# Kernel tuning notes

Measured on AMD Instinct MI355X. Metric: run time of the kernel, lower is better.

Reference implementation:

```python
import jax, jax.numpy as jnp
import numpy as np

B, H, N, T = 16, 16, 4096, 8
D_S, D_ID, L, K = 256, 128, 8, 32
HS, DQ = 8, 32
D_HID = 1024
D_STEER = 3 * D_S + D_ID  # cat(s_cur, id_cur, walker_state, token_embed)


def _gelu(x):
    return jax.nn.gelu(x, approximate=False)


def _rms(x, w):
    return x * jax.lax.rsqrt(jnp.mean(x * x, axis=-1, keepdims=True) + 1e-6) * w


def _mlp2(x, w1, b1, w2, b2):
    return _gelu(x @ w1 + b1) @ w2 + b2


def _per_plane_mlp(x, plane_idx, W1, b1, W2, b2):
    # x: [n, D_in]; plane_idx: [n] int in [0,L). Vectorized plane dispatch:
    # compute all planes then select (avoids data-dependent masking).
    h_all = jnp.einsum('nd,phd->nph', x, W1) + b1[None]          # [n,L,D_hid]
    h = jnp.take_along_axis(h_all, plane_idx[:, None, None], axis=1)[:, 0]
    h = _gelu(h)
    o_all = jnp.einsum('nh,pdh->npd', h, W2) + b2[None]          # [n,L,D_out]
    return jnp.take_along_axis(o_all, plane_idx[:, None, None], axis=1)[:, 0]


def setup_inputs() -> dict:
    key = jax.random.key(0)
    ks = jax.random.split(key, 16)
    f = jax.random.normal
    return {
        's': f(ks[0], (B, N, D_S), jnp.float32),
        'node_id': f(ks[1], (N, D_ID), jnp.float32),
        'walker_state': f(ks[2], (B, H, D_S), jnp.float32),
        'token_embed': f(ks[3], (B, T, D_S), jnp.float32),
        'norm_w': jnp.ones((D_S,), jnp.float32),
        'W1': f(ks[4], (L, D_HID, D_STEER), jnp.float32) * 0.014,
        'b1': jnp.zeros((L, D_HID), jnp.float32),
        'W2': f(ks[5], (L, D_S, D_HID), jnp.float32) * (2.0 / D_HID) ** 0.5,
        'b2': jnp.zeros((L, D_S), jnp.float32),
        'qw1': f(ks[6], (D_STEER, 2 * HS * DQ), jnp.float32) * 0.014,
        'qb1': jnp.zeros((2 * HS * DQ,), jnp.float32),
        'qw2': f(ks[7], (2 * HS * DQ, HS * DQ), jnp.float32) * 0.02,
        'qb2': jnp.zeros((HS * DQ,), jnp.float32),
        'kw1': f(ks[8], (D_ID, 2 * HS * DQ), jnp.float32) * 0.014,
        'kb1': jnp.zeros((2 * HS * DQ,), jnp.float32),
        'kw2': f(ks[9], (2 * HS * DQ, HS * DQ), jnp.float32) * 0.02,
        'kb2': jnp.zeros((HS * DQ,), jnp.float32),
        'walker_pos': jax.random.randint(ks[10], (B, H), 0, N, jnp.int32),
        'plane_idx': jax.random.randint(ks[11], (B, H), 0, L, jnp.int32),
        'neighbors': jax.random.randint(ks[12], (N, K), 0, N, jnp.int32),
    }


def reference(s, node_id, walker_state, token_embed, norm_w, W1, b1, W2, b2,
              qw1, qb1, qw2, qb2, kw1, kb1, kw2, kb2,
              walker_pos, plane_idx, neighbors):
    b_idx = jnp.arange(B)[:, None]            # [B,1] batch gather index
    plane_flat = plane_idx.reshape(-1)        # [B*H], constant per walker
    scale = 1.0 / (HS * np.sqrt(DQ).astype(np.float32))

    def step(carry, tok):
        s, pos, wstate, co, vc, lb = carry
        s_cur = s[b_idx, pos]                 # gather [B,H,D_s]
        id_cur = node_id[pos]                 # [B,H,D_id]
        s_n = _rms(s_cur, norm_w)
        tok_b = jnp.broadcast_to(tok[:, None, :], (B, H, D_S))
        steer = jnp.concatenate([s_n, id_cur, wstate, tok_b], axis=-1)  # [B,H,D_steer]
        # per-plane content MLP (dispatch by plane index)
        content = _per_plane_mlp(steer.reshape(B * H, D_STEER), plane_flat,
                                 W1, b1, W2, b2).reshape(B, H, D_S)
        # shared q/k projections and neighbor scoring
        q = _mlp2(steer, qw1, qb1, qw2, qb2).reshape(B, H, HS, DQ)
        nbr = neighbors[pos]                  # [B,H,K]
        k = _mlp2(node_id[nbr], kw1, kb1, kw2, kb2).reshape(B, H, K, HS, DQ)
        scores = jnp.einsum('bhsd,bhksd->bhk', q, k) * scale   # [B,H,K]
        probs = jax.nn.softmax(scores, axis=-1)
        mp = probs.mean(axis=(0, 1))
        lb = lb + K * jnp.sum(mp * mp)        # load-balance penalty
        # non-differentiable hop: argmax move
        sel = jnp.argmax(scores, axis=-1)     # [B,H]
        next_pos = jnp.take_along_axis(nbr, sel[..., None], axis=-1)[..., 0]
        # state updates: scatter content into s, residual walker state
        s_new = s.at[b_idx, pos].add(content)
        wstate_new = wstate + content
        # non-grad co-visit / visit-count accumulators
        pf = pos.reshape(-1)
        nf = next_pos.reshape(-1)
        co = co.at[pf, nf].add(1.0)
        vc = vc.at[nf].add(1.0)
        motor = wstate_new.mean(axis=1)       # [B,D_s]
        return (s_new, next_pos, wstate_new, co, vc, lb), motor

    init = (s, walker_pos, walker_state,
            jnp.zeros((N, N), jnp.float32), jnp.zeros((N,), jnp.float32),
            jnp.float32(0.0))
    (s_new, pos_new, ws_new, co, vc, lb), motors = jax.lax.scan(
        step, init, token_embed.transpose(1, 0, 2))
    motor_bt = motors.transpose(1, 0, 2)      # [B,T,D_s]
    return motor_bt, s_new, pos_new, ws_new, co, vc, lb
```

## Files before the change

### kernel.cpp

```cpp
#include <hip/hip_runtime.h>
#include <math.h>

#define B_    16
#define H_    16
#define N_    4096
#define T_    8
#define DS_   256
#define DID_  128
#define L_    8
#define K_    32
#define DHID_ 1024
#define DSTEER_ 896
#define QH_   512
#define QO_   256
#define NW_   256
#define SLOTS_ 512
#define SCORE_SCALE 0.022097086912079608f

struct KArgs {
    const float *s_in, *node_id, *ws_in, *token, *norm_w;
    const float *W1, *b1, *W2, *b2;
    const float *qw1, *qb1, *qw2, *qb2, *kw1, *kb1, *kw2, *kb2;
    const int *walker_pos, *plane_idx, *neighbors;
    float *out_motor, *out_s, *out_pos, *out_ws, *out_co, *out_vc, *out_lb;
    float *keys, *kh, *steer, *steerT, *h1p, *q1p, *c2p, *q2p, *mp_all;
    int *pos, *plane_order, *chunk_plane, *chunk_rows, *slot_of, *nchunks;
};

__device__ __forceinline__ float gelu_exact(float x) {
    return 0.5f * x * (1.0f + erff(x * 0.70710678118654752f));
}

#define FMA4(c, b, a) { c.x = fmaf(b.x, (a), c.x); c.y = fmaf(b.y, (a), c.y); \
                        c.z = fmaf(b.z, (a), c.z); c.w = fmaf(b.w, (a), c.w); }

__device__ __forceinline__ void gelu4(float4& v) {
    v.x = gelu_exact(v.x); v.y = gelu_exact(v.y);
    v.z = gelu_exact(v.z); v.w = gelu_exact(v.w);
}

__device__ __forceinline__ void rgemm_inner(
    const float* __restrict__ a0, const float* __restrict__ a1,
    const float* bp, int ldb, int K,
    float4& c0, float4& c1)
{
    for (int k = 0; k < K; k += 8) {
        const float4 a0l = *reinterpret_cast<const float4*>(a0 + k);
        const float4 a0h = *reinterpret_cast<const float4*>(a0 + k + 4);
        const float4 a1l = *reinterpret_cast<const float4*>(a1 + k);
        const float4 a1h = *reinterpret_cast<const float4*>(a1 + k + 4);
        const float* b8 = bp + (size_t)k * ldb;
#define KSTEP(o, av0, av1) { float4 bv = *reinterpret_cast<const float4*>(b8 + (size_t)(o) * ldb); \
                             FMA4(c0, bv, av0); FMA4(c1, bv, av1); }
        KSTEP(0, a0l.x, a1l.x)
        KSTEP(1, a0l.y, a1l.y)
        KSTEP(2, a0l.z, a1l.z)
        KSTEP(3, a0l.w, a1l.w)
        KSTEP(4, a0h.x, a1h.x)
        KSTEP(5, a0h.y, a1h.y)
        KSTEP(6, a0h.z, a1h.z)
        KSTEP(7, a0h.w, a1h.w)
#undef KSTEP
    }
}


__global__ __launch_bounds__(256) void setup1_kernel(KArgs a)
{
    int bid = blockIdx.x, tid = threadIdx.x;
    if (bid < 1024) {
        int u = bid;
        int rt = u >> 3, ct = u & 7;
        int tr = tid >> 4, tc = tid & 15;
        int row = rt * 32 + tr * 2, col = ct * 64 + tc * 4;
        const float* a0 = a.node_id + (size_t)row * DID_;
        float4 c0 = {0.f,0.f,0.f,0.f}, c1 = {0.f,0.f,0.f,0.f};
        rgemm_inner(a0, a0 + DID_, a.kw1 + col, QH_, DID_, c0, c1);
        float4 bv = *reinterpret_cast<const float4*>(a.kb1 + col);
        c0.x += bv.x; c0.y += bv.y; c0.z += bv.z; c0.w += bv.w;
        c1.x += bv.x; c1.y += bv.y; c1.z += bv.z; c1.w += bv.w;
        gelu4(c0); gelu4(c1);
        *reinterpret_cast<float4*>(a.kh + (size_t)row * QH_ + col) = c0;
        *reinterpret_cast<float4*>(a.kh + (size_t)(row + 1) * QH_ + col) = c1;
    } else if (bid == 1024) {
        a.pos[tid] = a.walker_pos[tid];
        a.mp_all[tid] = 0.f;
        __shared__ int cnt_s[8];
        __shared__ int cplane_s[16], cbase_s[16];
        __shared__ int nch_s;
        int wave = tid >> 6, lane = tid & 63;
        for (int pp = wave; pp < 8; pp += 4) {
            int base = 0;
            for (int c0 = 0; c0 < NW_; c0 += 64) {
                int w = c0 + lane;
                bool hit = (a.plane_idx[w] == pp);
                unsigned long long mask = __ballot(hit);
                if (hit) {
                    int rank = __popcll(mask & ((1ull << lane) - 1ull));
                    a.plane_order[pp * NW_ + base + rank] = w;
                }
                base += __popcll(mask);
            }
            if (lane == 0) cnt_s[pp] = base;
        }
        __syncthreads();
        if (tid == 0) {
            int nc = 0;
            for (int p = 0; p < 8; ++p)
                for (int s0 = 0; s0 < cnt_s[p]; s0 += 32) {
                    cplane_s[nc] = p; cbase_s[nc] = s0; ++nc;
                }
            *a.nchunks = nc;
            nch_s = nc;
        }
        __syncthreads();
        int nc = nch_s;
        for (int idx = tid; idx < 512; idx += 256) {
            int c = idx >> 5, i = idx & 31;
            int v = -1;
            if (c < nc) {
                int p = cplane_s[c];
                int r = cbase_s[c] + i;
                if (r < cnt_s[p]) v = a.plane_order[p * NW_ + r];
            }
            a.chunk_rows[c * 32 + i] = v;
            if (v >= 0) a.slot_of[v] = c * 32 + i;
            if (i == 0) a.chunk_plane[c] = (c < nc) ? cplane_s[c] : 0;
        }
    } else {
        int gid = (bid - 1025) * 256 + tid, stride = 2048 * 256;
        float4* s4o = reinterpret_cast<float4*>(a.out_s);
        const float4* s4i = reinterpret_cast<const float4*>(a.s_in);
        for (int i = gid; i < 4194304; i += stride) s4o[i] = s4i[i];
        float4* w4o = reinterpret_cast<float4*>(a.out_ws);
        const float4* w4i = reinterpret_cast<const float4*>(a.ws_in);
        for (int i = gid; i < 16384; i += stride) w4o[i] = w4i[i];
    }
}


__device__ void dev_steer(const KArgs& a, int w, int tid, int t) {
    int b = w >> 4;
    int p = a.pos[w];
    int slot = a.slot_of[w];
    float sc = a.out_s[((size_t)b * N_ + p) * DS_ + tid];
    float v = sc * sc;
    for (int off = 32; off > 0; off >>= 1) v += __shfl_down(v, off);
    __shared__ float red[4];
    if ((tid & 63) == 0) red[tid >> 6] = v;
    __syncthreads();
    float tot = red[0] + red[1] + red[2] + red[3];
    float r = rsqrtf(tot * (1.0f / DS_) + 1e-6f);
    float* st = a.steer + (size_t)w * DSTEER_;
    float v0 = sc * r * a.norm_w[tid];
    float v2 = a.out_ws[(size_t)w * DS_ + tid];
    float v3 = a.token[((size_t)b * T_ + t) * DS_ + tid];
    st[tid] = v0;
    st[384 + tid] = v2;
    st[640 + tid] = v3;
    a.steerT[(size_t)tid * SLOTS_ + slot] = v0;
    a.steerT[(size_t)(384 + tid) * SLOTS_ + slot] = v2;
    a.steerT[(size_t)(640 + tid) * SLOTS_ + slot] = v3;
    if (tid < 128) {
        float v1 = a.node_id[(size_t)p * DID_ + tid];
        st[256 + tid] = v1;
        a.steerT[(size_t)(256 + tid) * SLOTS_ + slot] = v1;
    }
}


__global__ __launch_bounds__(256) void setup2_kernel(KArgs a)
{
    int bid = blockIdx.x, tid = threadIdx.x;
    if (bid < 512) {
        int rt = bid >> 2, ct = bid & 3;
        int tr = tid >> 4, tc = tid & 15;
        int row = rt * 32 + tr * 2, col = ct * 64 + tc * 4;
        const float* a0 = a.kh + (size_t)row * QH_;
        float4 c0 = {0.f,0.f,0.f,0.f}, c1 = {0.f,0.f,0.f,0.f};
        rgemm_inner(a0, a0 + QH_, a.kw2 + col, QO_, QH_, c0, c1);
        float4 bv = *reinterpret_cast<const float4*>(a.kb2 + col);
        c0.x += bv.x; c0.y += bv.y; c0.z += bv.z; c0.w += bv.w;
        c1.x += bv.x; c1.y += bv.y; c1.z += bv.z; c1.w += bv.w;
        *reinterpret_cast<float4*>(a.keys + (size_t)row * QO_ + col) = c0;
        *reinterpret_cast<float4*>(a.keys + (size_t)(row + 1) * QO_ + col) = c1;
    } else {
        dev_steer(a, bid - 512, tid, 0);
    }
}

__global__ __launch_bounds__(256) void steer_kernel(KArgs a, int t)
{
    dev_steer(a, blockIdx.x, threadIdx.x, t);
}


__global__ __launch_bounds__(256) void l1_kernel(KArgs a)
{
    __shared__ float bs[224 * 32];
    int bid = blockIdx.x, tid = threadIdx.x;
    int tr = tid >> 3, tc = tid & 7;
    float4 c0 = {0.f,0.f,0.f,0.f}, c1 = {0.f,0.f,0.f,0.f};
    if (bid < 256) {
        int kp = bid & 3, tile = bid >> 2;
        int rt = tile >> 4, ct = tile & 15;
        int row = rt * 64 + tr * 2, col0 = ct * 32;
#pragma unroll
        for (int i = 0; i < 7; ++i) {
            int idx = tid + i * 256;
            int kk = idx >> 3, c4 = (idx & 7) << 2;
            *reinterpret_cast<float4*>(bs + kk * 32 + c4) =
                *reinterpret_cast<const float4*>(a.qw1 + (size_t)(kp * 224 + kk) * QH_ + col0 + c4);
        }
        __syncthreads();
        const float* a0 = a.steer + (size_t)row * DSTEER_ + kp * 224;
        rgemm_inner(a0, a0 + DSTEER_, bs + tc * 4, 32, 224, c0, c1);
        float* o = a.q1p + (size_t)kp * 131072;
        int col = col0 + tc * 4;
        *reinterpret_cast<float4*>(o + (size_t)row * QH_ + col) = c0;
        *reinterpret_cast<float4*>(o + (size_t)(row + 1) * QH_ + col) = c1;
    } else {
        int b2 = bid - 256;
        int kp = b2 & 3, tile = b2 >> 2;
        int c = tile >> 4, jt = tile & 15;
        if (c >= *a.nchunks) return;
        int p = a.chunk_plane[c];
        int J = jt * 64 + tr * 2;
#pragma unroll
        for (int i = 0; i < 7; ++i) {
            int idx = tid + i * 256;
            int kk = idx >> 3, s4 = (idx & 7) << 2;
            *reinterpret_cast<float4*>(bs + kk * 32 + s4) =
                *reinterpret_cast<const float4*>(a.steerT + (size_t)(kp * 224 + kk) * SLOTS_ + c * 32 + s4);
        }
        __syncthreads();
        const float* a0 = a.W1 + ((size_t)p * DHID_ + J) * DSTEER_ + kp * 224;
        rgemm_inner(a0, a0 + DSTEER_, bs + tc * 4, 32, 224, c0, c1);
        float* o = a.h1p + (size_t)kp * 524288;
        int slot = c * 32 + tc * 4;
        *reinterpret_cast<float4*>(o + (size_t)J * SLOTS_ + slot) = c0;
        *reinterpret_cast<float4*>(o + (size_t)(J + 1) * SLOTS_ + slot) = c1;
    }
}


__global__ __launch_bounds__(256) void l2f_kernel(KArgs a)
{
    __shared__ float smem[4096];
    int bid = blockIdx.x, tid = threadIdx.x;
    if (bid < 256) {
        int kp = bid & 7, tile = bid >> 3;
        int rt = tile >> 2, ct = tile & 3;
        int tr = tid >> 4, tc = tid & 15;
        int row0 = rt * 32, col = ct * 64 + tc * 4;
        float4 c0 = {0.f,0.f,0.f,0.f}, c1 = {0.f,0.f,0.f,0.f};
#pragma unroll
        for (int i = 0; i < 2; ++i) {
            int idx = tid + i * 256;
            int r = idx >> 4, k4 = (idx & 15) << 2;
            size_t off = (size_t)(row0 + r) * QH_ + kp * 64 + k4;
            float4 acc = *reinterpret_cast<const float4*>(a.qb1 + kp * 64 + k4);
#pragma unroll
            for (int p4 = 0; p4 < 4; ++p4) {
                float4 v = *reinterpret_cast<const float4*>(a.q1p + (size_t)p4 * 131072 + off);
                acc.x += v.x; acc.y += v.y; acc.z += v.z; acc.w += v.w;
            }
            gelu4(acc);
            *reinterpret_cast<float4*>(smem + r * 72 + k4) = acc;
        }
        __syncthreads();
        const float* a0 = smem + (tr * 2) * 72;
        rgemm_inner(a0, a0 + 72, a.qw2 + (size_t)(kp * 64) * QO_ + col, QO_, 64, c0, c1);
        float* o = a.q2p + (size_t)kp * 65536;
        int row = row0 + tr * 2;
        *reinterpret_cast<float4*>(o + (size_t)row * QO_ + col) = c0;
        *reinterpret_cast<float4*>(o + (size_t)(row + 1) * QO_ + col) = c1;
    } else {
        int b2i = bid - 256;
        int kp = b2i & 7, tile = b2i >> 3;
        int c = tile >> 2, jt = tile & 3;
        if (c >= *a.nchunks) return;
        int p = a.chunk_plane[c];
        int tr = tid >> 3, tc = tid & 7;
        int J = jt * 64 + tr * 2;
        float4 c0 = {0.f,0.f,0.f,0.f}, c1 = {0.f,0.f,0.f,0.f};
#pragma unroll
        for (int i = 0; i < 4; ++i) {
            int idx = tid + i * 256;
            int kk = idx >> 3, s4 = (idx & 7) << 2;
            int kq = kp * 128 + kk;
            size_t off = (size_t)kq * SLOTS_ + c * 32 + s4;
            float bj = a.b1[p * DHID_ + kq];
            float4 acc = {bj, bj, bj, bj};
#pragma unroll
            for (int p4 = 0; p4 < 4; ++p4) {
                float4 v = *reinterpret_cast<const float4*>(a.h1p + (size_t)p4 * 524288 + off);
                acc.x += v.x; acc.y += v.y; acc.z += v.z; acc.w += v.w;
            }
            gelu4(acc);
            *reinterpret_cast<float4*>(smem + kk * 32 + s4) = acc;
        }
        __syncthreads();
        const float* a0 = a.W2 + ((size_t)p * DS_ + J) * DHID_ + kp * 128;
        rgemm_inner(a0, a0 + DHID_, smem + tc * 4, 32, 128, c0, c1);
        __syncthreads();
        int jl = tr * 2;
        smem[(tc*4+0)*66 + jl]     = c0.x;
        smem[(tc*4+1)*66 + jl]     = c0.y;
        smem[(tc*4+2)*66 + jl]     = c0.z;
        smem[(tc*4+3)*66 + jl]     = c0.w;
        smem[(tc*4+0)*66 + jl + 1] = c1.x;
        smem[(tc*4+1)*66 + jl + 1] = c1.y;
        smem[(tc*4+2)*66 + jl + 1] = c1.z;
        smem[(tc*4+3)*66 + jl + 1] = c1.w;
        __syncthreads();
        float* o = a.c2p + (size_t)kp * 131072;
#pragma unroll
        for (int i = 0; i < 2; ++i) {
            int f4i = tid + i * 256;
            int sl = f4i >> 4, j4 = (f4i & 15) << 2;
            float4 v;
            v.x = smem[sl * 66 + j4 + 0];
            v.y = smem[sl * 66 + j4 + 1];
            v.z = smem[sl * 66 + j4 + 2];
            v.w = smem[sl * 66 + j4 + 3];
            *reinterpret_cast<float4*>(o + (size_t)(c * 32 + sl) * 256 + jt * 64 + j4) = v;
        }
    }
}


__global__ __launch_bounds__(256) void score_kernel(KArgs a, int t)
{
    int w = blockIdx.x;
    int b = w >> 4;
    int tid = threadIdx.x;
    int pold = a.pos[w];
    int slot = a.slot_of[w];
    __shared__ float qv_s[256];
    __shared__ int nbr_s[32];
    __shared__ float part_s[8][32];
    __shared__ float sc_s[32];
    if (tid < 32) nbr_s[tid] = a.neighbors[(size_t)pold * K_ + tid];
    float qsum = a.qb2[tid];
#pragma unroll
    for (int kp = 0; kp < 8; ++kp) qsum += a.q2p[(size_t)kp * 65536 + (size_t)w * QO_ + tid];
    qv_s[tid] = qsum;
    float csum = a.b2[a.chunk_plane[slot >> 5] * DS_ + tid];
#pragma unroll
    for (int kp = 0; kp < 8; ++kp) csum += a.c2p[(size_t)kp * 131072 + (size_t)slot * 256 + tid];
    __syncthreads();
    int k = tid & 31, part = tid >> 5;
    int nk = nbr_s[k];
    const float* kp_ = a.keys + (size_t)nk * 256 + part * 32;
    const float* qp = qv_s + part * 32;
    float acc = 0.f;
#pragma unroll
    for (int i = 0; i < 32; i += 4) {
        float4 kv = *reinterpret_cast<const float4*>(kp_ + i);
        acc += kv.x * qp[i] + kv.y * qp[i+1] + kv.z * qp[i+2] + kv.w * qp[i+3];
    }
    part_s[part][k] = acc;
    __syncthreads();
    if (tid < 32) {
        float s = 0.f;
#pragma unroll
        for (int p8 = 0; p8 < 8; ++p8) s += part_s[p8][tid];
        sc_s[tid] = s * SCORE_SCALE;
    }
    __syncthreads();
    if (tid < 32) {
        float sv = sc_s[tid];
        float m = sv;
        for (int off = 1; off < 32; off <<= 1) m = fmaxf(m, __shfl_xor(m, off));
        float e = expf(sv - m);
        float ssum = e;
        for (int off = 1; off < 32; off <<= 1) ssum += __shfl_xor(ssum, off);
        float prob = e / ssum;
        atomicAdd(&a.mp_all[t * 32 + tid], prob);
        float bs = sv; int bi = tid;
        for (int off = 1; off < 32; off <<= 1) {
            float os = __shfl_xor(bs, off);
            int   oi = __shfl_xor(bi, off);
            if (os > bs || (os == bs && oi < bi)) { bs = os; bi = oi; }
        }
        if (tid == 0) {
            int next = nbr_s[bi];
            a.pos[w] = next;
            if (t == T_ - 1) a.out_pos[w] = (float)next;
            atomicAdd(&a.out_co[(size_t)pold * N_ + next], 1.0f);
            atomicAdd(&a.out_vc[next], 1.0f);
        }
    }
    atomicAdd(&a.out_s[((size_t)b * N_ + pold) * DS_ + tid], csum);
    float wn = a.out_ws[(size_t)w * DS_ + tid] + csum;
    a.out_ws[(size_t)w * DS_ + tid] = wn;
    atomicAdd(&a.out_motor[((size_t)b * T_ + t) * DS_ + tid], wn * (1.0f / H_));
}

__global__ __launch_bounds__(256) void final_kernel(KArgs a)
{
    int tid = threadIdx.x;
    float v = a.mp_all[tid] * (1.0f / 256.f);
    v = v * v;
    for (int off = 32; off > 0; off >>= 1) v += __shfl_down(v, off);
    __shared__ float red[4];
    if ((tid & 63) == 0) red[tid >> 6] = v;
    __syncthreads();
    if (tid == 0) a.out_lb[0] = (float)K_ * (red[0] + red[1] + red[2] + red[3]);
}


extern "C" void kernel_launch(void* const* d_in, const int* in_sizes, int n_in,
                              void* d_out, int out_size, void* d_ws, size_t ws_size,
                              hipStream_t stream)
{
    KArgs a;
    a.s_in    = (const float*)d_in[0];
    a.node_id = (const float*)d_in[1];
    a.ws_in   = (const float*)d_in[2];
    a.token   = (const float*)d_in[3];
    a.norm_w  = (const float*)d_in[4];
    a.W1  = (const float*)d_in[5];
    a.b1  = (const float*)d_in[6];
    a.W2  = (const float*)d_in[7];
    a.b2  = (const float*)d_in[8];
    a.qw1 = (const float*)d_in[9];
    a.qb1 = (const float*)d_in[10];
    a.qw2 = (const float*)d_in[11];
    a.qb2 = (const float*)d_in[12];
    a.kw1 = (const float*)d_in[13];
    a.kb1 = (const float*)d_in[14];
    a.kw2 = (const float*)d_in[15];
    a.kb2 = (const float*)d_in[16];
    a.walker_pos = (const int*)d_in[17];
    a.plane_idx  = (const int*)d_in[18];
    a.neighbors  = (const int*)d_in[19];

    float* out = (float*)d_out;
    a.out_motor = out;
    a.out_s     = a.out_motor + 32768;
    a.out_pos   = a.out_s + (size_t)16777216;
    a.out_ws    = a.out_pos + 256;
    a.out_co    = a.out_ws + 65536;
    a.out_vc    = a.out_co + (size_t)16777216;
    a.out_lb    = a.out_vc + 4096;

    float* ws = (float*)d_ws;
    a.keys   = ws;
    a.steer  = a.keys + 1048576;
    a.steerT = a.steer + 229376;
    a.h1p    = a.steerT + 458752;
    a.kh     = a.h1p;
    a.q1p    = a.h1p + 2097152;
    a.c2p    = a.q1p + 524288;
    a.q2p    = a.c2p + 1048576;
    a.mp_all = a.q2p + 524288;
    a.pos         = (int*)(a.mp_all + 256);
    a.plane_order = a.pos + 256;
    a.chunk_plane = a.plane_order + 2048;
    a.chunk_rows  = a.chunk_plane + 16;
    a.slot_of     = a.chunk_rows + 512;
    a.nchunks     = a.slot_of + 256;

    hipMemsetAsync(a.out_motor, 0, 32768 * sizeof(float), stream);
    hipMemsetAsync(a.out_co, 0, (size_t)(16777216 + 4096 + 1) * sizeof(float), stream);

    setup1_kernel<<<1024 + 1 + 2048, 256, 0, stream>>>(a);
    setup2_kernel<<<512 + 256, 256, 0, stream>>>(a);
    for (int t = 0; t < T_; ++t) {
        l1_kernel<<<256 + 1024, 256, 0, stream>>>(a);
        l2f_kernel<<<768, 256, 0, stream>>>(a);
        score_kernel<<<256, 256, 0, stream>>>(a, t);
        if (t < T_ - 1) steer_kernel<<<256, 256, 0, stream>>>(a, t + 1);
    }
    final_kernel<<<1, 256, 0, stream>>>(a);
}
```

Measured before the change: 502.2 us.

## Fuse steer construction into l1 kernel and pre-transpose query weights

Removes the separate steer kernel, dropping one launch per step. The l1 blocks now gather s, node_id, walker state and token rows themselves and compute the RMS norm inline, writing the steer tile into padded shared memory. The qw1 and qw2 weights are transposed once in setup, so the query GEMMs can stream weights as the A operand with steer/hidden as B. Each l1 block now redoes the gather and norm work, and l2f adds a shared-memory transpose before its stores.

Result: faster. 485.9 us (-3.2%).

```diff
diff --git a/kernel.cpp b/kernel.cpp
--- a/kernel.cpp
+++ b/kernel.cpp
@@ -15,6 +15,7 @@
 #define QO_   256
 #define NW_   256
 #define SLOTS_ 512
+#define BSLD_ 36
 #define SCORE_SCALE 0.022097086912079608f
 
 struct KArgs {
@@ -23,7 +24,7 @@
     const float *qw1, *qb1, *qw2, *qb2, *kw1, *kb1, *kw2, *kb2;
     const int *walker_pos, *plane_idx, *neighbors;
     float *out_motor, *out_s, *out_pos, *out_ws, *out_co, *out_vc, *out_lb;
-    float *keys, *kh, *steer, *steerT, *h1p, *q1p, *c2p, *q2p, *mp_all;
+    float *keys, *kh, *qw1T, *qw2T, *h1p, *q1p, *c2p, *q2p, *mp_all;
     int *pos, *plane_order, *chunk_plane, *chunk_rows, *slot_of, *nchunks;
 };
 
@@ -127,8 +128,33 @@
             if (v >= 0) a.slot_of[v] = c * 32 + i;
             if (i == 0) a.chunk_plane[c] = (c < nc) ? cplane_s[c] : 0;
         }
+    } else if (bid < 1601) {
+        __shared__ float ts[32][33];
+        int u = bid - 1025;
+        const float* src; float* dst; int srcld, dstld, td, tj;
+        if (u < 448) {
+            src = a.qw1; dst = a.qw1T; srcld = QH_; dstld = DSTEER_;
+            td = u >> 4; tj = u & 15;
+        } else {
+            u -= 448;
+            src = a.qw2; dst = a.qw2T; srcld = QO_; dstld = QH_;
+            td = u >> 3; tj = u & 7;
+        }
+#pragma unroll
+        for (int i = 0; i < 4; ++i) {
+            int e = tid + i * 256;
+            int r = e >> 5, cc = e & 31;
+            ts[r][cc] = src[(size_t)(td * 32 + r) * srcld + tj * 32 + cc];
+        }
+        __syncthreads();
+#pragma unroll
+        for (int i = 0; i < 4; ++i) {
+            int e = tid + i * 256;
+            int r = e >> 5, cc = e & 31;
+            dst[(size_t)(tj * 32 + r) * dstld + td * 32 + cc] = ts[cc][r];
+        }
     } else {
-        int gid = (bid - 1025) * 256 + tid, stride = 2048 * 256;
+        int gid = (bid - 1601) * 256 + tid, stride = 2048 * 256;
         float4* s4o = reinterpret_cast<float4*>(a.out_s);
         const float4* s4i = reinterpret_cast<const float4*>(a.s_in);
         for (int i = gid; i < 4194304; i += stride) s4o[i] = s4i[i];
@@ -139,103 +165,115 @@
 }
 
 
-__device__ void dev_steer(const KArgs& a, int w, int tid, int t) {
-    int b = w >> 4;
-    int p = a.pos[w];
-    int slot = a.slot_of[w];
-    float sc = a.out_s[((size_t)b * N_ + p) * DS_ + tid];
-    float v = sc * sc;
-    for (int off = 32; off > 0; off >>= 1) v += __shfl_down(v, off);
-    __shared__ float red[4];
-    if ((tid & 63) == 0) red[tid >> 6] = v;
-    __syncthreads();
-    float tot = red[0] + red[1] + red[2] + red[3];
-    float r = rsqrtf(tot * (1.0f / DS_) + 1e-6f);
-    float* st = a.steer + (size_t)w * DSTEER_;
-    float v0 = sc * r * a.norm_w[tid];
-    float v2 = a.out_ws[(size_t)w * DS_ + tid];
-    float v3 = a.token[((size_t)b * T_ + t) * DS_ + tid];
-    st[tid] = v0;
-    st[384 + tid] = v2;
-    st[640 + tid] = v3;
-    a.steerT[(size_t)tid * SLOTS_ + slot] = v0;
-    a.steerT[(size_t)(384 + tid) * SLOTS_ + slot] = v2;
-    a.steerT[(size_t)(640 + tid) * SLOTS_ + slot] = v3;
-    if (tid < 128) {
-        float v1 = a.node_id[(size_t)p * DID_ + tid];
-        st[256 + tid] = v1;
-        a.steerT[(size_t)(256 + tid) * SLOTS_ + slot] = v1;
-    }
-}
-
-
 __global__ __launch_bounds__(256) void setup2_kernel(KArgs a)
 {
     int bid = blockIdx.x, tid = threadIdx.x;
-    if (bid < 512) {
-        int rt = bid >> 2, ct = bid & 3;
-        int tr = tid >> 4, tc = tid & 15;
-        int row = rt * 32 + tr * 2, col = ct * 64 + tc * 4;
-        const float* a0 = a.kh + (size_t)row * QH_;
-        float4 c0 = {0.f,0.f,0.f,0.f}, c1 = {0.f,0.f,0.f,0.f};
-        rgemm_inner(a0, a0 + QH_, a.kw2 + col, QO_, QH_, c0, c1);
-        float4 bv = *reinterpret_cast<const float4*>(a.kb2 + col);
-        c0.x += bv.x; c0.y += bv.y; c0.z += bv.z; c0.w += bv.w;
-        c1.x += bv.x; c1.y += bv.y; c1.z += bv.z; c1.w += bv.w;
-        *reinterpret_cast<float4*>(a.keys + (size_t)row * QO_ + col) = c0;
-        *reinterpret_cast<float4*>(a.keys + (size_t)(row + 1) * QO_ + col) = c1;
+    int rt = bid >> 2, ct = bid & 3;
+    int tr = tid >> 4, tc = tid & 15;
+    int row = rt * 32 + tr * 2, col = ct * 64 + tc * 4;
+    const float* a0 = a.kh + (size_t)row * QH_;
+    float4 c0 = {0.f,0.f,0.f,0.f}, c1 = {0.f,0.f,0.f,0.f};
+    rgemm_inner(a0, a0 + QH_, a.kw2 + col, QO_, QH_, c0, c1);
+    float4 bv = *reinterpret_cast<const float4*>(a.kb2 + col);
+    c0.x += bv.x; c0.y += bv.y; c0.z += bv.z; c0.w += bv.w;
+    c1.x += bv.x; c1.y += bv.y; c1.z += bv.z; c1.w += bv.w;
+    *reinterpret_cast<float4*>(a.keys + (size_t)row * QO_ + col) = c0;
+    *reinterpret_cast<float4*>(a.keys + (size_t)(row + 1) * QO_ + col) = c1;
+}
+
+
+__global__ __launch_bounds__(256) void l1_kernel(KArgs a, int t)
+{
+    __shared__ float bs[224 * BSLD_];
+    __shared__ float rms_s[32];
+    __shared__ int w_s[32], pos_s[32];
+    int bid = blockIdx.x, tid = threadIdx.x;
+    int kp, jt, c = -1, p = 0, wt = 0, isQ;
+    if (bid < 256) {
+        isQ = 1; kp = bid & 3;
+        int tile = bid >> 2;
+        wt = tile >> 3; jt = tile & 7;
     } else {
-        dev_steer(a, bid - 512, tid, 0);
-    }
-}
-
-__global__ __launch_bounds__(256) void steer_kernel(KArgs a, int t)
-{
-    dev_steer(a, blockIdx.x, threadIdx.x, t);
-}
-
-
-__global__ __launch_bounds__(256) void l1_kernel(KArgs a)
-{
-    __shared__ float bs[224 * 32];
-    int bid = blockIdx.x, tid = threadIdx.x;
+        isQ = 0;
+        int b2 = bid - 256; kp = b2 & 3;
+        int tile = b2 >> 2;
+        c = tile >> 4; jt = tile & 15;
+        if (c >= *a.nchunks) return;
+        p = a.chunk_plane[c];
+    }
+    int g = tid >> 3, l8 = tid & 7;
+    if (l8 == 0) {
+        int w = isQ ? (wt * 32 + g) : a.chunk_rows[c * 32 + g];
+        w_s[g] = w;
+        pos_s[g] = (w >= 0) ? a.pos[w] : 0;
+    }
+    __syncthreads();
+    if (kp < 2) {
+        int w = w_s[g];
+        float ssum = 0.f;
+        if (w >= 0) {
+            const float* sr = a.out_s + ((size_t)(w >> 4) * N_ + pos_s[g]) * DS_ + l8 * 32;
+#pragma unroll
+            for (int i = 0; i < 8; ++i) {
+                float4 v = *reinterpret_cast<const float4*>(sr + i * 4);
+                ssum += v.x * v.x + v.y * v.y + v.z * v.z + v.w * v.w;
+            }
+        }
+        ssum += __shfl_xor(ssum, 1);
+        ssum += __shfl_xor(ssum, 2);
+        ssum += __shfl_xor(ssum, 4);
+        if (l8 == 0) rms_s[g] = rsqrtf(ssum * (1.0f / DS_) + 1e-6f);
+    }
+    __syncthreads();
+    {
+        int w = w_s[g];
+        int b = (w >= 0) ? (w >> 4) : 0;
+        int pp = pos_s[g];
+        float rr = (kp < 2) ? rms_s[g] : 0.f;
+#pragma unroll
+        for (int i = 0; i < 7; ++i) {
+            int kk = l8 * 28 + i * 4;
+            int d4 = kp * 224 + kk;
+            float4 v = make_float4(0.f, 0.f, 0.f, 0.f);
+            if (w >= 0) {
+                if (d4 < 256) {
+                    float4 sv = *reinterpret_cast<const float4*>(
+                        a.out_s + ((size_t)b * N_ + pp) * DS_ + d4);
+                    float4 nv = *reinterpret_cast<const float4*>(a.norm_w + d4);
+                    v.x = sv.x * rr * nv.x; v.y = sv.y * rr * nv.y;
+                    v.z = sv.z * rr * nv.z; v.w = sv.w * rr * nv.w;
+                } else if (d4 < 384) {
+                    v = *reinterpret_cast<const float4*>(
+                        a.node_id + (size_t)pp * DID_ + (d4 - 256));
+                } else if (d4 < 640) {
+                    v = *reinterpret_cast<const float4*>(
+                        a.out_ws + (size_t)w * DS_ + (d4 - 384));
+                } else {
+                    v = *reinterpret_cast<const float4*>(
+                        a.token + ((size_t)b * T_ + t) * DS_ + (d4 - 640));
+                }
+            }
+            bs[(kk + 0) * BSLD_ + g] = v.x;
+            bs[(kk + 1) * BSLD_ + g] = v.y;
+            bs[(kk + 2) * BSLD_ + g] = v.z;
+            bs[(kk + 3) * BSLD_ + g] = v.w;
+        }
+    }
+    __syncthreads();
     int tr = tid >> 3, tc = tid & 7;
     float4 c0 = {0.f,0.f,0.f,0.f}, c1 = {0.f,0.f,0.f,0.f};
-    if (bid < 256) {
-        int kp = bid & 3, tile = bid >> 2;
-        int rt = tile >> 4, ct = tile & 15;
-        int row = rt * 64 + tr * 2, col0 = ct * 32;
-#pragma unroll
-        for (int i = 0; i < 7; ++i) {
-            int idx = tid + i * 256;
-            int kk = idx >> 3, c4 = (idx & 7) << 2;
-            *reinterpret_cast<float4*>(bs + kk * 32 + c4) =
-                *reinterpret_cast<const float4*>(a.qw1 + (size_t)(kp * 224 + kk) * QH_ + col0 + c4);
-        }
-        __syncthreads();
-        const float* a0 = a.steer + (size_t)row * DSTEER_ + kp * 224;
-        rgemm_inner(a0, a0 + DSTEER_, bs + tc * 4, 32, 224, c0, c1);
+    if (isQ) {
+        int j = jt * 64 + tr * 2;
+        const float* a0 = a.qw1T + (size_t)j * DSTEER_ + kp * 224;
+        rgemm_inner(a0, a0 + DSTEER_, bs + tc * 4, BSLD_, 224, c0, c1);
         float* o = a.q1p + (size_t)kp * 131072;
-        int col = col0 + tc * 4;
-        *reinterpret_cast<float4*>(o + (size_t)row * QH_ + col) = c0;
-        *reinterpret_cast<float4*>(o + (size_t)(row + 1) * QH_ + col) = c1;
+        int w4 = wt * 32 + tc * 4;
+        *reinterpret_cast<float4*>(o + (size_t)j * NW_ + w4) = c0;
+        *reinterpret_cast<float4*>(o + (size_t)(j + 1) * NW_ + w4) = c1;
     } else {
-        int b2 = bid - 256;
-        int kp = b2 & 3, tile = b2 >> 2;
-        int c = tile >> 4, jt = tile & 15;
-        if (c >= *a.nchunks) return;
-        int p = a.chunk_plane[c];
         int J = jt * 64 + tr * 2;
-#pragma unroll
-        for (int i = 0; i < 7; ++i) {
-            int idx = tid + i * 256;
-            int kk = idx >> 3, s4 = (idx & 7) << 2;
-            *reinterpret_cast<float4*>(bs + kk * 32 + s4) =
-                *reinterpret_cast<const float4*>(a.steerT + (size_t)(kp * 224 + kk) * SLOTS_ + c * 32 + s4);
-        }
-        __syncthreads();
         const float* a0 = a.W1 + ((size_t)p * DHID_ + J) * DSTEER_ + kp * 224;
-        rgemm_inner(a0, a0 + DSTEER_, bs + tc * 4, 32, 224, c0, c1);
+        rgemm_inner(a0, a0 + DSTEER_, bs + tc * 4, BSLD_, 224, c0, c1);
         float* o = a.h1p + (size_t)kp * 524288;
         int slot = c * 32 + tc * 4;
         *reinterpret_cast<float4*>(o + (size_t)J * SLOTS_ + slot) = c0;
@@ -246,35 +284,50 @@
 
 __global__ __launch_bounds__(256) void l2f_kernel(KArgs a)
 {
-    __shared__ float smem[4096];
+    __shared__ float smem[4224];
     int bid = blockIdx.x, tid = threadIdx.x;
     if (bid < 256) {
         int kp = bid & 7, tile = bid >> 3;
-        int rt = tile >> 2, ct = tile & 3;
-        int tr = tid >> 4, tc = tid & 15;
-        int row0 = rt * 32, col = ct * 64 + tc * 4;
+        int colt = tile >> 3, wt = tile & 7;
+#pragma unroll
+        for (int i = 0; i < 8; ++i) {
+            int idx = tid + i * 256;
+            int hh = idx >> 5, wl = idx & 31;
+            size_t off = (size_t)(kp * 64 + hh) * NW_ + wt * 32 + wl;
+            float acc = a.qb1[kp * 64 + hh];
+#pragma unroll
+            for (int p4 = 0; p4 < 4; ++p4) acc += a.q1p[(size_t)p4 * 131072 + off];
+            smem[hh * 32 + wl] = gelu_exact(acc);
+        }
+        __syncthreads();
+        int tr = tid >> 3, tc = tid & 7;
+        int col = colt * 64 + tr * 2;
+        const float* a0 = a.qw2T + (size_t)col * QH_ + kp * 64;
         float4 c0 = {0.f,0.f,0.f,0.f}, c1 = {0.f,0.f,0.f,0.f};
+        rgemm_inner(a0, a0 + QH_, smem + tc * 4, 32, 64, c0, c1);
+        __syncthreads();
+        int cl = tr * 2;
+        smem[(tc*4+0)*66 + cl]     = c0.x;
+        smem[(tc*4+1)*66 + cl]     = c0.y;
+        smem[(tc*4+2)*66 + cl]     = c0.z;
+        smem[(tc*4+3)*66 + cl]     = c0.w;
+        smem[(tc*4+0)*66 + cl + 1] = c1.x;
+        smem[(tc*4+1)*66 + cl + 1] = c1.y;
+        smem[(tc*4+2)*66 + cl + 1] = c1.z;
+        smem[(tc*4+3)*66 + cl + 1] = c1.w;
+        __syncthreads();
+        float* o = a.q2p + (size_t)kp * 65536;
 #pragma unroll
         for (int i = 0; i < 2; ++i) {
-            int idx = tid + i * 256;
-            int r = idx >> 4, k4 = (idx & 15) << 2;
-            size_t off = (size_t)(row0 + r) * QH_ + kp * 64 + k4;
-            float4 acc = *reinterpret_cast<const float4*>(a.qb1 + kp * 64 + k4);
-#pragma unroll
-            for (int p4 = 0; p4 < 4; ++p4) {
-                float4 v = *reinterpret_cast<const float4*>(a.q1p + (size_t)p4 * 131072 + off);
-                acc.x += v.x; acc.y += v.y; acc.z += v.z; acc.w += v.w;
-            }
-            gelu4(acc);
-            *reinterpret_cast<float4*>(smem + r * 72 + k4) = acc;
-        }
-        __syncthreads();
-        const float* a0 = smem + (tr * 2) * 72;
-        rgemm_inner(a0, a0 + 72, a.qw2 + (size_t)(kp * 64) * QO_ + col, QO_, 64, c0, c1);
-        float* o = a.q2p + (size_t)kp * 65536;
-        int row = row0 + tr * 2;
-        *reinterpret_cast<float4*>(o + (size_t)row * QO_ + col) = c0;
-        *reinterpret_cast<float4*>(o + (size_t)(row + 1) * QO_ + col) = c1;
+            int f4i = tid + i * 256;
+            int wl = f4i >> 4, j4 = (f4i & 15) << 2;
+            float4 v;
+            v.x = smem[wl * 66 + j4 + 0];
+            v.y = smem[wl * 66 + j4 + 1];
+            v.z = smem[wl * 66 + j4 + 2];
+            v.w = smem[wl * 66 + j4 + 3];
+            *reinterpret_cast<float4*>(o + (size_t)(wt * 32 + wl) * QO_ + colt * 64 + j4) = v;
+        }
     } else {
         int b2i = bid - 256;
         int kp = b2i & 7, tile = b2i >> 3;
@@ -448,9 +501,9 @@
 
     float* ws = (float*)d_ws;
     a.keys   = ws;
-    a.steer  = a.keys + 1048576;
-    a.steerT = a.steer + 229376;
-    a.h1p    = a.steerT + 458752;
+    a.qw1T   = a.keys + 1048576;
+    a.qw2T   = a.qw1T + 458752;
+    a.h1p    = a.qw2T + 131072;
     a.kh     = a.h1p;
     a.q1p    = a.h1p + 2097152;
     a.c2p    = a.q1p + 524288;
@@ -466,13 +519,12 @@
     hipMemsetAsync(a.out_motor, 0, 32768 * sizeof(float), stream);
     hipMemsetAsync(a.out_co, 0, (size_t)(16777216 + 4096 + 1) * sizeof(float), stream);
 
-    setup1_kernel<<<1024 + 1 + 2048, 256, 0, stream>>>(a);
-    setup2_kernel<<<512 + 256, 256, 0, stream>>>(a);
+    setup1_kernel<<<1024 + 1 + 576 + 2048, 256, 0, stream>>>(a);
+    setup2_kernel<<<512, 256, 0, stream>>>(a);
     for (int t = 0; t < T_; ++t) {
-        l1_kernel<<<256 + 1024, 256, 0, stream>>>(a);
+        l1_kernel<<<256 + 1024, 256, 0, stream>>>(a, t);
         l2f_kernel<<<768, 256, 0, stream>>>(a);
         score_kernel<<<256, 256, 0, stream>>>(a, t);
-        if (t < T_ - 1) steer_kernel<<<256, 256, 0, stream>>>(a, t + 1);
     }
     final_kernel<<<1, 256, 0, stream>>>(a);
 }
```
